# Kernel tuning notes

Measured on AMD Instinct MI355X. Metric: run time of the kernel, lower is better.

The kernel has to match this reference:

```python
import jax, jax.numpy as jnp
import numpy as np

N, FIN, FOUT = 4096, 256, 256


def setup_inputs() -> dict:
    key = jax.random.key(0)
    ks = jax.random.split(key, 6)
    x = jax.random.normal(ks[0], (N, FIN), jnp.float32)
    adj = jax.random.randint(ks[1], (N, N), 0, 2, jnp.int32)  # dense 0/1 adjacency
    W = jax.random.normal(ks[2], (FOUT, FIN), jnp.float32) / np.sqrt(FIN)
    b = jax.random.normal(ks[3], (FOUT,), jnp.float32) * 0.01
    att_w = jax.random.normal(ks[4], (2 * FOUT,), jnp.float32) / np.sqrt(2.0 * FOUT)  # Linear(2F,1).weight squeezed
    att_b = jax.random.normal(ks[5], (), jnp.float32) * 0.01
    return {"x": x, "adj": adj, "W": W, "b": b, "att_w": att_w, "att_b": att_b}


def reference(x, adj, W, b, att_w, att_b):
    n = x.shape[0]
    fo = W.shape[0]
    h = x @ W.T + b  # [N, Fout]
    # score(i,j) = att([h_i ; h_j]) = h_i.w1 + h_j.w2 + att_b  -> no [N,N,2F] concat
    s = (h @ att_w[:fo])[:, None] + (h @ att_w[fo:])[None, :] + att_b  # [N, N]
    edge = adj == 1
    # GLOBAL softmax over all edges (faithful to F.softmax(stacked_scores, dim=0))
    gmax = jnp.max(jnp.where(edge, s, -jnp.inf))
    e = jnp.exp(s - gmax)
    denom = jnp.sum(jnp.where(edge, e, 0.0))
    p = (e / denom).reshape(-1)  # softmaxed score per pair (valid at edges)
    # original indexes attention_scores[j] by NODE id j into the row-major edge list:
    # recover the score of the j-th global edge (j = 0..N-1) via cumsum rank + scatter
    flat = edge.reshape(-1)
    rank = jnp.cumsum(flat.astype(jnp.int32)) - 1  # rank of each edge in row-major order
    idx = jnp.where(flat, rank, n)  # non-edges and ranks >= n get dropped
    w_node = jnp.zeros((n,), h.dtype).at[idx].set(p, mode="drop")  # [N]
    # output[i] = sum_{j: adj[i,j]==1} w_node[j] * h[j]
    out = jax.nn.relu(edge.astype(h.dtype) @ (w_node[:, None] * h))
    return out
```

## Files before the change

### kernel.cpp

```cpp
#include <hip/hip_runtime.h>
#include <cstdint>
#include <cstddef>

#define NN 4096
#define FDIM 256

typedef __attribute__((ext_vector_type(4))) float fx4;
typedef __attribute__((ext_vector_type(8))) short s8v;

__device__ inline uint16_t f2bf(float f) {
    union { float f; uint32_t u; } v; v.f = f;
    const uint32_t u = v.u;
    return (uint16_t)((u + 0x7FFFu + ((u >> 16) & 1u)) >> 16);
}

__global__ __launch_bounds__(512, 4) void k_h(const float* __restrict__ x,
        const float* __restrict__ W, const float* __restrict__ bias,
        const float* __restrict__ att_w, uint16_t* __restrict__ gt,
        float* __restrict__ a1p, float* __restrict__ a2p) {
    __shared__ __align__(16) float xs[2][64 * 68];
    __shared__ __align__(16) float wt[2][64 * 68];
    const int bi = blockIdx.x, bf = blockIdx.y;
    const int t = threadIdx.x;
    const int t256 = t & 255;
    const int kh = t >> 8;
    const int tx = t256 & 15, ty = t256 >> 4;
    float acc[4][4] = {};
    float rx[8], rw[8];
    #pragma unroll
    for (int u = 0; u < 8; ++u) {
        const int e = t + 512 * u, r = e >> 6, c = e & 63;
        rx[u] = x[(size_t)(bi * 64 + r) * 256 + c];
        rw[u] = W[(size_t)(bf * 64 + r) * 256 + c];
    }
    for (int p = 0; p < 4; ++p) {
        float* xb = xs[p & 1];
        float* wb = wt[p & 1];
        #pragma unroll
        for (int u = 0; u < 8; ++u) {
            const int e = t + 512 * u, r = e >> 6, c = e & 63;
            const int sw = 8 * ((c & 7) ^ ((c >> 3) & 7));
            xb[c * 68 + (r ^ sw)] = rx[u];
            wb[c * 68 + (r ^ sw)] = rw[u];
        }
        __syncthreads();
        if (p < 3) {
            const int kc = (p + 1) * 64;
            #pragma unroll
            for (int u = 0; u < 8; ++u) {
                const int e = t + 512 * u, r = e >> 6, c = e & 63;
                rx[u] = x[(size_t)(bi * 64 + r) * 256 + kc + c];
                rw[u] = W[(size_t)(bf * 64 + r) * 256 + kc + c];
            }
        }
        #pragma unroll 8
        for (int k = 0; k < 32; ++k) {
            const int kk = kh * 32 + k;
            const int sw = 8 * ((kk & 7) ^ ((kk >> 3) & 7));
            const fx4 av = *(const fx4*)(xb + kk * 68 + ((ty * 4) ^ sw));
            const fx4 bv = *(const fx4*)(wb + kk * 68 + ((tx * 4) ^ sw));
            #pragma unroll
            for (int u = 0; u < 4; ++u)
                #pragma unroll
                for (int v = 0; v < 4; ++v)
                    acc[u][v] += av[u] * bv[v];
        }
    }
    __syncthreads();
    float* cbuf = xs[0];
    if (kh == 1) {
        #pragma unroll
        for (int u = 0; u < 4; ++u)
            *(fx4*)(cbuf + t256 * 16 + u * 4) = *(const fx4*)(&acc[u][0]);
    }
    __syncthreads();
    if (kh == 0) {
        float* tileT = wt[0];
        #pragma unroll
        for (int u = 0; u < 4; ++u) {
            const fx4 o = *(const fx4*)(cbuf + t256 * 16 + u * 4);
            #pragma unroll
            for (int v = 0; v < 4; ++v) acc[u][v] += o[v];
        }
        const fx4 bv = *(const fx4*)(bias + bf * 64 + tx * 4);
        const fx4 w1v = *(const fx4*)(att_w + bf * 64 + tx * 4);
        const fx4 w2v = *(const fx4*)(att_w + 256 + bf * 64 + tx * 4);
        #pragma unroll
        for (int u = 0; u < 4; ++u) {
            const int i = bi * 64 + ty * 4 + u;
            fx4 r;
            float s1 = 0.f, s2 = 0.f;
            #pragma unroll
            for (int v = 0; v < 4; ++v) {
                r[v] = acc[u][v] + bv[v];
                s1 += r[v] * w1v[v];
                s2 += r[v] * w2v[v];
            }
            #pragma unroll
            for (int v = 0; v < 4; ++v)
                tileT[(tx * 4 + v) * 68 + ty * 4 + u] = r[v];
            #pragma unroll
            for (int d = 8; d > 0; d >>= 1) {
                s1 += __shfl_down(s1, d, 16);
                s2 += __shfl_down(s2, d, 16);
            }
            if (tx == 0) {
                a1p[bf * NN + i] = s1;
                a2p[bf * NN + i] = s2;
            }
        }
    }
    __syncthreads();
    {
        const float* tileT = wt[0];
        const int fl = t >> 3, cb = t & 7;
        const int pcb = cb ^ (fl & 7);
        s8v v;
        #pragma unroll
        for (int lo = 0; lo < 8; ++lo)
            v[lo] = (short)f2bf(tileT[fl * 68 + cb * 8 + lo]);
        *(s8v*)(gt + (size_t)(bf * 64 + fl) * NN + bi * 64 + pcb * 8) = v;
    }
}

__global__ __launch_bounds__(1024) void k_prep(const float* __restrict__ a1p,
        const float* __restrict__ a2p, const int* __restrict__ adj,
        float* __restrict__ E1, float* __restrict__ E2,
        float* __restrict__ wraw, float* __restrict__ Sg) {
    __shared__ float E1s[NN];
    __shared__ float E2s[NN];
    __shared__ float red1[16], red2[16];
    __shared__ int wtot[16];
    __shared__ int base_s;
    const int t = threadIdx.x, lane = t & 63, wv = t >> 6;
    fx4 v1 = {0.f, 0.f, 0.f, 0.f}, v2 = {0.f, 0.f, 0.f, 0.f};
    #pragma unroll
    for (int bf = 0; bf < 4; ++bf) {
        v1 += *(const fx4*)(a1p + bf * NN + t * 4);
        v2 += *(const fx4*)(a2p + bf * NN + t * 4);
    }
    float m1 = fmaxf(fmaxf(v1[0], v1[1]), fmaxf(v1[2], v1[3]));
    float m2 = fmaxf(fmaxf(v2[0], v2[1]), fmaxf(v2[2], v2[3]));
    #pragma unroll
    for (int d = 32; d > 0; d >>= 1) {
        m1 = fmaxf(m1, __shfl_down(m1, d));
        m2 = fmaxf(m2, __shfl_down(m2, d));
    }
    if (lane == 0) { red1[wv] = m1; red2[wv] = m2; }
    __syncthreads();
    if (t == 0) {
        float mm1 = -1e30f, mm2 = -1e30f;
        for (int k = 0; k < 16; ++k) {
            mm1 = fmaxf(mm1, red1[k]);
            mm2 = fmaxf(mm2, red2[k]);
        }
        red1[0] = mm1; red2[0] = mm2;
        *Sg = 0.f;
        base_s = 0;
    }
    __syncthreads();
    const float M1 = red1[0], M2 = red2[0];
    fx4 e1v, e2v, z4 = {0.f, 0.f, 0.f, 0.f};
    #pragma unroll
    for (int j = 0; j < 4; ++j) {
        e1v[j] = expf(v1[j] - M1);
        e2v[j] = expf(v2[j] - M2);
    }
    *(fx4*)(E1s + t * 4) = e1v;
    *(fx4*)(E2s + t * 4) = e2v;
    *(fx4*)(E1 + t * 4) = e1v;
    *(fx4*)(E2 + t * 4) = e2v;
    *(fx4*)(wraw + t * 4) = z4;
    __syncthreads();
    for (int row = 0; row < NN; ++row) {
        const int base = base_s;
        if (base >= NN) break;
        const int4 a = ((const int4*)(adj + (size_t)row * NN))[t];
        const int vj[4] = {a.x, a.y, a.z, a.w};
        int cnt = 0;
        #pragma unroll
        for (int j = 0; j < 4; ++j) cnt += (vj[j] == 1);
        int inc = cnt;
        #pragma unroll
        for (int d = 1; d < 64; d <<= 1) {
            const int y = __shfl_up(inc, d);
            if (lane >= d) inc += y;
        }
        if (lane == 63) wtot[wv] = inc;
        __syncthreads();
        int wbase = 0, total = 0;
        #pragma unroll
        for (int w = 0; w < 16; ++w) {
            const int xw = wtot[w];
            total += xw;
            wbase += (w < wv) ? xw : 0;
        }
        if (t == 0) base_s = base + total;
        int r = base + wbase + inc - cnt;
        if (cnt && r < NN) {
            const float e1 = E1s[row];
            #pragma unroll
            for (int j = 0; j < 4; ++j) {
                if (vj[j] == 1) {
                    if (r < NN) wraw[r] = e1 * E2s[t * 4 + j];
                    ++r;
                }
            }
        }
        __syncthreads();
    }
}

__global__ __launch_bounds__(256, 3) void k_fused(const int* __restrict__ adj,
        const uint16_t* __restrict__ gt, const float* __restrict__ E1,
        const float* __restrict__ E2, const float* __restrict__ wraw,
        uint16_t* __restrict__ part, float* __restrict__ Sg, int krange) {
    __shared__ __align__(16) uint16_t As[64 * 72];
    __shared__ __align__(16) uint16_t Gs[256 * 64];
    __shared__ float sgred[4];
    const int ib = blockIdx.x, ks = blockIdx.y;
    const int t = threadIdx.x;
    const int wv = t >> 6, lane = t & 63;
    const int q = lane >> 4, m16 = lane & 15;
    const int i0 = ib * 64, k0 = ks * krange;
    const int ksteps = krange >> 6;
    const int ar = t >> 4, ac4 = (t & 15) * 4;
    const int fr = lane >> 3, cb = lane & 7;
    fx4 acc[4][4];
    #pragma unroll
    for (int a = 0; a < 4; ++a)
        #pragma unroll
        for (int b2 = 0; b2 < 4; ++b2) acc[a][b2] = (fx4){0.f, 0.f, 0.f, 0.f};
    float sS = 0.f;
    float e1r[4];
    #pragma unroll
    for (int p = 0; p < 4; ++p) e1r[p] = E1[i0 + p * 16 + ar];
    int4 ra[4];
    #pragma unroll
    for (int p = 0; p < 4; ++p)
        ra[p] = *(const int4*)(adj + (size_t)(i0 + p * 16 + ar) * NN + k0 + ac4);
    fx4 rw4 = *(const fx4*)(wraw + k0 + ac4);
    fx4 re2 = *(const fx4*)(E2 + k0 + ac4);

    for (int stp = 0; stp < ksteps; ++stp) {
        const int kk = k0 + stp * 64;
        const uint16_t wb0 = f2bf(rw4[0]), wb1 = f2bf(rw4[1]);
        const uint16_t wb2 = f2bf(rw4[2]), wb3 = f2bf(rw4[3]);
        #pragma unroll
        for (int p = 0; p < 4; ++p) {
            uint2 wo;
            wo.x = (ra[p].x == 1 ? (uint32_t)wb0 : 0u) |
                   ((ra[p].y == 1 ? (uint32_t)wb1 : 0u) << 16);
            wo.y = (ra[p].z == 1 ? (uint32_t)wb2 : 0u) |
                   ((ra[p].w == 1 ? (uint32_t)wb3 : 0u) << 16);
            *(uint2*)(&As[(p * 16 + ar) * 72 + ac4]) = wo;
            sS += e1r[p] * ((ra[p].x == 1 ? re2[0] : 0.f) +
                            (ra[p].y == 1 ? re2[1] : 0.f) +
                            (ra[p].z == 1 ? re2[2] : 0.f) +
                            (ra[p].w == 1 ? re2[3] : 0.f));
        }
        #pragma unroll
        for (int p = 0; p < 8; ++p) {
            const int f0 = wv * 64 + p * 8;
            const uint16_t* gp = gt + (size_t)(f0 + fr) * NN + kk + cb * 8;
            __builtin_amdgcn_global_load_lds(
                (const __attribute__((address_space(1))) uint32_t*)gp,
                (__attribute__((address_space(3))) uint32_t*)(Gs + f0 * 64),
                16, 0, 0);
        }
        __syncthreads();
        if (stp + 1 < ksteps) {
            #pragma unroll
            for (int p = 0; p < 4; ++p)
                ra[p] = *(const int4*)(adj + (size_t)(i0 + p * 16 + ar) * NN +
                                       kk + 64 + ac4);
            rw4 = *(const fx4*)(wraw + kk + 64 + ac4);
            re2 = *(const fx4*)(E2 + kk + 64 + ac4);
        }
        s8v afr[4][2];
        #pragma unroll
        for (int it = 0; it < 4; ++it)
            #pragma unroll
            for (int khh = 0; khh < 2; ++khh)
                afr[it][khh] = *(const s8v*)(As + (it * 16 + m16) * 72 + khh * 32 + q * 8);
        #pragma unroll
        for (int ft = 0; ft < 4; ++ft) {
            #pragma unroll
            for (int khh = 0; khh < 2; ++khh) {
                const int row = wv * 64 + ft * 16 + m16;
                const int pcb = ((khh << 2) | q) ^ (m16 & 7);
                const s8v bfr = *(const s8v*)(Gs + row * 64 + pcb * 8);
                #pragma unroll
                for (int it = 0; it < 4; ++it)
                    acc[it][ft] = __builtin_amdgcn_mfma_f32_16x16x32_bf16(
                        afr[it][khh], bfr, acc[it][ft], 0, 0, 0);
            }
        }
        __syncthreads();
    }
    #pragma unroll
    for (int d = 32; d > 0; d >>= 1) sS += __shfl_down(sS, d);
    if (lane == 0) sgred[wv] = sS;
    __syncthreads();
    if (t == 0)
        atomicAdd(Sg, sgred[0] + sgred[1] + sgred[2] + sgred[3]);
    uint16_t* dst = part + (size_t)ks * NN * FDIM;
    #pragma unroll
    for (int it = 0; it < 4; ++it) {
        #pragma unroll
        for (int ft = 0; ft < 4; ++ft) {
            const int f = wv * 64 + ft * 16 + m16;
            #pragma unroll
            for (int r = 0; r < 4; ++r) {
                const int i = i0 + it * 16 + q * 4 + r;
                dst[(size_t)i * FDIM + f] = f2bf(acc[it][ft][r]);
            }
        }
    }
}

__global__ __launch_bounds__(256) void k_out(const uint16_t* __restrict__ part,
        const float* __restrict__ Sg, float* __restrict__ out, int nsplit) {
    const size_t idx = ((size_t)blockIdx.x * 256 + threadIdx.x) * 8;
    const float inv = 1.0f / (*Sg);
    float s[8] = {};
    for (int k = 0; k < nsplit; ++k) {
        const s8v v = *(const s8v*)(part + (size_t)k * NN * FDIM + idx);
        #pragma unroll
        for (int j = 0; j < 8; ++j) {
            union { uint32_t u; float f; } cv;
            cv.u = ((uint32_t)(uint16_t)v[j]) << 16;
            s[j] += cv.f;
        }
    }
    fx4 r0, r1;
    #pragma unroll
    for (int j = 0; j < 4; ++j) {
        r0[j] = fmaxf(s[j], 0.f) * inv;
        r1[j] = fmaxf(s[4 + j], 0.f) * inv;
    }
    *(fx4*)(out + idx) = r0;
    *(fx4*)(out + idx + 4) = r1;
}

extern "C" void kernel_launch(void* const* d_in, const int* in_sizes, int n_in,
                              void* d_out, int out_size, void* d_ws, size_t ws_size,
                              hipStream_t stream) {
    const float* x     = (const float*)d_in[0];
    const int*   adj   = (const int*)d_in[1];
    const float* W     = (const float*)d_in[2];
    const float* bias  = (const float*)d_in[3];
    const float* att_w = (const float*)d_in[4];
    float* out = (float*)d_out;
    char* ws = (char*)d_ws;
    uint16_t* gt   = (uint16_t*)(ws + 0);
    float*    a1p  = (float*)(ws + 2097152);
    float*    a2p  = (float*)(ws + 2162688);
    float*    E1   = (float*)(ws + 2228224);
    float*    E2   = (float*)(ws + 2244608);
    float*    wraw = (float*)(ws + 2260992);
    float*    Sg   = (float*)(ws + 2277376);
    uint16_t* part = (uint16_t*)(ws + 2277632);
    (void)in_sizes; (void)n_in; (void)out_size;

    const size_t avail = (ws_size > 2277632) ? (ws_size - 2277632) : 0;
    int splitk = 1;
    while (splitk < 8 &&
           (size_t)(splitk * 2) * NN * FDIM * sizeof(uint16_t) <= avail)
        splitk <<= 1;
    const int krange = NN / splitk;

    k_h    <<<dim3(64, 4), 512, 0, stream>>>(x, W, bias, att_w, gt, a1p, a2p);
    k_prep <<<dim3(1), 1024, 0, stream>>>(a1p, a2p, adj, E1, E2, wraw, Sg);
    k_fused<<<dim3(64, splitk), 256, 0, stream>>>(adj, gt, E1, E2, wraw, part, Sg, krange);
    k_out  <<<dim3(512), 256, 0, stream>>>(part, Sg, out, splitk);
}
```

Measured before the change: 148.1 us.

## Load B operand directly into registers and double-buffer adjacency tile in LDS

The fused aggregation kernel stops staging the transposed feature tile through LDS via global_load_lds and instead loads each wave's B fragments straight from global memory into registers, prefetching the next step. The adjacency-weight A tile is double-buffered in LDS so the trailing barrier per step is removed, and adjacency rows are prefetched two steps ahead. The XOR swizzle on the gt writes is dropped since the LDS bank-conflict layout is no longer needed. This raises register pressure, so occupancy is lowered to 2 blocks per CU. It also assumes ksteps is even.

After: 153.2 us. 1.03x slower.

```diff
diff --git a/kernel.cpp b/kernel.cpp
--- a/kernel.cpp
+++ b/kernel.cpp
@@ -114,12 +114,11 @@
     {
         const float* tileT = wt[0];
         const int fl = t >> 3, cb = t & 7;
-        const int pcb = cb ^ (fl & 7);
         s8v v;
         #pragma unroll
         for (int lo = 0; lo < 8; ++lo)
             v[lo] = (short)f2bf(tileT[fl * 68 + cb * 8 + lo]);
-        *(s8v*)(gt + (size_t)(bf * 64 + fl) * NN + bi * 64 + pcb * 8) = v;
+        *(s8v*)(gt + (size_t)(bf * 64 + fl) * NN + bi * 64 + cb * 8) = v;
     }
 }
 
@@ -211,12 +210,11 @@
     }
 }
 
-__global__ __launch_bounds__(256, 3) void k_fused(const int* __restrict__ adj,
+__global__ __launch_bounds__(256, 2) void k_fused(const int* __restrict__ adj,
         const uint16_t* __restrict__ gt, const float* __restrict__ E1,
         const float* __restrict__ E2, const float* __restrict__ wraw,
         uint16_t* __restrict__ part, float* __restrict__ Sg, int krange) {
-    __shared__ __align__(16) uint16_t As[64 * 72];
-    __shared__ __align__(16) uint16_t Gs[256 * 64];
+    __shared__ __align__(16) uint16_t As[2][64 * 72];
     __shared__ float sgred[4];
     const int ib = blockIdx.x, ks = blockIdx.y;
     const int t = threadIdx.x;
@@ -225,7 +223,6 @@
     const int i0 = ib * 64, k0 = ks * krange;
     const int ksteps = krange >> 6;
     const int ar = t >> 4, ac4 = (t & 15) * 4;
-    const int fr = lane >> 3, cb = lane & 7;
     fx4 acc[4][4];
     #pragma unroll
     for (int a = 0; a < 4; ++a)
@@ -235,69 +232,83 @@
     float e1r[4];
     #pragma unroll
     for (int p = 0; p < 4; ++p) e1r[p] = E1[i0 + p * 16 + ar];
-    int4 ra[4];
+    const uint16_t* rowp[4];
+    #pragma unroll
+    for (int ft = 0; ft < 4; ++ft)
+        rowp[ft] = gt + (size_t)(wv * 64 + ft * 16 + m16) * NN + q * 8;
+
+    int4 ra0[4], ra1[4];
     #pragma unroll
     for (int p = 0; p < 4; ++p)
-        ra[p] = *(const int4*)(adj + (size_t)(i0 + p * 16 + ar) * NN + k0 + ac4);
-    fx4 rw4 = *(const fx4*)(wraw + k0 + ac4);
-    fx4 re2 = *(const fx4*)(E2 + k0 + ac4);
-
-    for (int stp = 0; stp < ksteps; ++stp) {
+        ra0[p] = *(const int4*)(adj + (size_t)(i0 + p * 16 + ar) * NN + k0 + ac4);
+    #pragma unroll
+    for (int p = 0; p < 4; ++p)
+        ra1[p] = *(const int4*)(adj + (size_t)(i0 + p * 16 + ar) * NN + k0 + 64 + ac4);
+    fx4 rwC = *(const fx4*)(wraw + k0 + ac4);
+    fx4 reC = *(const fx4*)(E2 + k0 + ac4);
+    s8v B0[4][2], B1[4][2];
+    #pragma unroll
+    for (int ft = 0; ft < 4; ++ft) {
+        B0[ft][0] = *(const s8v*)(rowp[ft] + k0);
+        B0[ft][1] = *(const s8v*)(rowp[ft] + k0 + 32);
+    }
+
+    auto step = [&](s8v (&Bc)[4][2], s8v (&Bn)[4][2], int4 (&Rc)[4], int stp) {
+        const int cur = stp & 1;
         const int kk = k0 + stp * 64;
-        const uint16_t wb0 = f2bf(rw4[0]), wb1 = f2bf(rw4[1]);
-        const uint16_t wb2 = f2bf(rw4[2]), wb3 = f2bf(rw4[3]);
+        const uint16_t wb0 = f2bf(rwC[0]), wb1 = f2bf(rwC[1]);
+        const uint16_t wb2 = f2bf(rwC[2]), wb3 = f2bf(rwC[3]);
         #pragma unroll
         for (int p = 0; p < 4; ++p) {
             uint2 wo;
-            wo.x = (ra[p].x == 1 ? (uint32_t)wb0 : 0u) |
-                   ((ra[p].y == 1 ? (uint32_t)wb1 : 0u) << 16);
-            wo.y = (ra[p].z == 1 ? (uint32_t)wb2 : 0u) |
-                   ((ra[p].w == 1 ? (uint32_t)wb3 : 0u) << 16);
-            *(uint2*)(&As[(p * 16 + ar) * 72 + ac4]) = wo;
-            sS += e1r[p] * ((ra[p].x == 1 ? re2[0] : 0.f) +
-                            (ra[p].y == 1 ? re2[1] : 0.f) +
-                            (ra[p].z == 1 ? re2[2] : 0.f) +
-                            (ra[p].w == 1 ? re2[3] : 0.f));
-        }
-        #pragma unroll
-        for (int p = 0; p < 8; ++p) {
-            const int f0 = wv * 64 + p * 8;
-            const uint16_t* gp = gt + (size_t)(f0 + fr) * NN + kk + cb * 8;
-            __builtin_amdgcn_global_load_lds(
-                (const __attribute__((address_space(1))) uint32_t*)gp,
-                (__attribute__((address_space(3))) uint32_t*)(Gs + f0 * 64),
-                16, 0, 0);
+            wo.x = (Rc[p].x == 1 ? (uint32_t)wb0 : 0u) |
+                   ((Rc[p].y == 1 ? (uint32_t)wb1 : 0u) << 16);
+            wo.y = (Rc[p].z == 1 ? (uint32_t)wb2 : 0u) |
+                   ((Rc[p].w == 1 ? (uint32_t)wb3 : 0u) << 16);
+            *(uint2*)(&As[cur][(p * 16 + ar) * 72 + ac4]) = wo;
+            sS += e1r[p] * ((Rc[p].x == 1 ? reC[0] : 0.f) +
+                            (Rc[p].y == 1 ? reC[1] : 0.f) +
+                            (Rc[p].z == 1 ? reC[2] : 0.f) +
+                            (Rc[p].w == 1 ? reC[3] : 0.f));
         }
         __syncthreads();
+        if (stp + 2 < ksteps) {
+            #pragma unroll
+            for (int p = 0; p < 4; ++p)
+                Rc[p] = *(const int4*)(adj + (size_t)(i0 + p * 16 + ar) * NN +
+                                       kk + 128 + ac4);
+        }
         if (stp + 1 < ksteps) {
-            #pragma unroll
-            for (int p = 0; p < 4; ++p)
-                ra[p] = *(const int4*)(adj + (size_t)(i0 + p * 16 + ar) * NN +
-                                       kk + 64 + ac4);
-            rw4 = *(const fx4*)(wraw + kk + 64 + ac4);
-            re2 = *(const fx4*)(E2 + kk + 64 + ac4);
+            rwC = *(const fx4*)(wraw + kk + 64 + ac4);
+            reC = *(const fx4*)(E2 + kk + 64 + ac4);
+            #pragma unroll
+            for (int ft = 0; ft < 4; ++ft) {
+                Bn[ft][0] = *(const s8v*)(rowp[ft] + kk + 64);
+                Bn[ft][1] = *(const s8v*)(rowp[ft] + kk + 64 + 32);
+            }
         }
         s8v afr[4][2];
         #pragma unroll
         for (int it = 0; it < 4; ++it)
             #pragma unroll
             for (int khh = 0; khh < 2; ++khh)
-                afr[it][khh] = *(const s8v*)(As + (it * 16 + m16) * 72 + khh * 32 + q * 8);
-        #pragma unroll
-        for (int ft = 0; ft < 4; ++ft) {
-            #pragma unroll
-            for (int khh = 0; khh < 2; ++khh) {
-                const int row = wv * 64 + ft * 16 + m16;
-                const int pcb = ((khh << 2) | q) ^ (m16 & 7);
-                const s8v bfr = *(const s8v*)(Gs + row * 64 + pcb * 8);
+                afr[it][khh] = *(const s8v*)(&As[cur][(it * 16 + m16) * 72 +
+                                                      khh * 32 + q * 8]);
+        #pragma unroll
+        for (int ft = 0; ft < 4; ++ft)
+            #pragma unroll
+            for (int khh = 0; khh < 2; ++khh)
                 #pragma unroll
                 for (int it = 0; it < 4; ++it)
                     acc[it][ft] = __builtin_amdgcn_mfma_f32_16x16x32_bf16(
-                        afr[it][khh], bfr, acc[it][ft], 0, 0, 0);
-            }
-        }
-        __syncthreads();
-    }
+                        afr[it][khh], Bc[ft][khh], acc[it][ft], 0, 0, 0);
+    };
+
+    for (int stp = 0; stp < ksteps; stp += 2) {
+        step(B0, B1, ra0, stp);
+        step(B1, B0, ra1, stp + 1);
+    }
+
     #pragma unroll
     for (int d = 32; d > 0; d >>= 1) sS += __shfl_down(sS, d);
     if (lane == 0) sgred[wv] = sS;
```

## Fuse single-block prep kernel into split-K fused kernel with redundant per-block edge ranking

Applied to the files above, without the earlier changes.

Removes the single-block k_prep kernel, which serially scanned adjacency rows to build the node weight vector. Each k_fused block now recomputes the global maxima, E1/E2 exponentials and its own slice of edge-rank weights in shared memory, stopping once enough edges have been counted. This removes a serial launch that used one block on the device. In exchange, every block redundantly scans early adjacency rows and reduces a1p/a2p, and the split-K factor is now fixed at 8 with no workspace-size check.

New measurement: 154.2 us. +4.1%, slower.

```diff
diff --git a/kernel.cpp b/kernel.cpp
--- a/kernel.cpp
+++ b/kernel.cpp
@@ -4,6 +4,9 @@
 
 #define NN 4096
 #define FDIM 256
+#define SPLITK 8
+#define KRANGE 512
+#define KSTEPS 8
 
 typedef __attribute__((ext_vector_type(4))) float fx4;
 typedef __attribute__((ext_vector_type(8))) short s8v;
@@ -17,7 +20,7 @@
 __global__ __launch_bounds__(512, 4) void k_h(const float* __restrict__ x,
         const float* __restrict__ W, const float* __restrict__ bias,
         const float* __restrict__ att_w, uint16_t* __restrict__ gt,
-        float* __restrict__ a1p, float* __restrict__ a2p) {
+        float* __restrict__ a1p, float* __restrict__ a2p, float* __restrict__ Sg) {
     __shared__ __align__(16) float xs[2][64 * 68];
     __shared__ __align__(16) float wt[2][64 * 68];
     const int bi = blockIdx.x, bf = blockIdx.y;
@@ -25,6 +28,7 @@
     const int t256 = t & 255;
     const int kh = t >> 8;
     const int tx = t256 & 15, ty = t256 >> 4;
+    if (bi == 0 && bf == 0 && t == 0) *Sg = 0.f;
     float acc[4][4] = {};
     float rx[8], rw[8];
     #pragma unroll
@@ -123,136 +127,140 @@
     }
 }
 
-__global__ __launch_bounds__(1024) void k_prep(const float* __restrict__ a1p,
-        const float* __restrict__ a2p, const int* __restrict__ adj,
-        float* __restrict__ E1, float* __restrict__ E2,
-        float* __restrict__ wraw, float* __restrict__ Sg) {
-    __shared__ float E1s[NN];
-    __shared__ float E2s[NN];
-    __shared__ float red1[16], red2[16];
-    __shared__ int wtot[16];
-    __shared__ int base_s;
-    const int t = threadIdx.x, lane = t & 63, wv = t >> 6;
-    fx4 v1 = {0.f, 0.f, 0.f, 0.f}, v2 = {0.f, 0.f, 0.f, 0.f};
-    #pragma unroll
-    for (int bf = 0; bf < 4; ++bf) {
-        v1 += *(const fx4*)(a1p + bf * NN + t * 4);
-        v2 += *(const fx4*)(a2p + bf * NN + t * 4);
-    }
-    float m1 = fmaxf(fmaxf(v1[0], v1[1]), fmaxf(v1[2], v1[3]));
-    float m2 = fmaxf(fmaxf(v2[0], v2[1]), fmaxf(v2[2], v2[3]));
-    #pragma unroll
-    for (int d = 32; d > 0; d >>= 1) {
-        m1 = fmaxf(m1, __shfl_down(m1, d));
-        m2 = fmaxf(m2, __shfl_down(m2, d));
-    }
-    if (lane == 0) { red1[wv] = m1; red2[wv] = m2; }
-    __syncthreads();
-    if (t == 0) {
-        float mm1 = -1e30f, mm2 = -1e30f;
-        for (int k = 0; k < 16; ++k) {
-            mm1 = fmaxf(mm1, red1[k]);
-            mm2 = fmaxf(mm2, red2[k]);
-        }
-        red1[0] = mm1; red2[0] = mm2;
-        *Sg = 0.f;
-        base_s = 0;
-    }
-    __syncthreads();
-    const float M1 = red1[0], M2 = red2[0];
-    fx4 e1v, e2v, z4 = {0.f, 0.f, 0.f, 0.f};
-    #pragma unroll
-    for (int j = 0; j < 4; ++j) {
-        e1v[j] = expf(v1[j] - M1);
-        e2v[j] = expf(v2[j] - M2);
-    }
-    *(fx4*)(E1s + t * 4) = e1v;
-    *(fx4*)(E2s + t * 4) = e2v;
-    *(fx4*)(E1 + t * 4) = e1v;
-    *(fx4*)(E2 + t * 4) = e2v;
-    *(fx4*)(wraw + t * 4) = z4;
-    __syncthreads();
-    for (int row = 0; row < NN; ++row) {
-        const int base = base_s;
-        if (base >= NN) break;
-        const int4 a = ((const int4*)(adj + (size_t)row * NN))[t];
-        const int vj[4] = {a.x, a.y, a.z, a.w};
-        int cnt = 0;
-        #pragma unroll
-        for (int j = 0; j < 4; ++j) cnt += (vj[j] == 1);
-        int inc = cnt;
-        #pragma unroll
-        for (int d = 1; d < 64; d <<= 1) {
-            const int y = __shfl_up(inc, d);
-            if (lane >= d) inc += y;
-        }
-        if (lane == 63) wtot[wv] = inc;
-        __syncthreads();
-        int wbase = 0, total = 0;
-        #pragma unroll
-        for (int w = 0; w < 16; ++w) {
-            const int xw = wtot[w];
-            total += xw;
-            wbase += (w < wv) ? xw : 0;
-        }
-        if (t == 0) base_s = base + total;
-        int r = base + wbase + inc - cnt;
-        if (cnt && r < NN) {
-            const float e1 = E1s[row];
-            #pragma unroll
-            for (int j = 0; j < 4; ++j) {
-                if (vj[j] == 1) {
-                    if (r < NN) wraw[r] = e1 * E2s[t * 4 + j];
-                    ++r;
-                }
-            }
-        }
-        __syncthreads();
-    }
-}
-
 __global__ __launch_bounds__(256, 3) void k_fused(const int* __restrict__ adj,
-        const uint16_t* __restrict__ gt, const float* __restrict__ E1,
-        const float* __restrict__ E2, const float* __restrict__ wraw,
-        uint16_t* __restrict__ part, float* __restrict__ Sg, int krange) {
+        const uint16_t* __restrict__ gt, const float* __restrict__ a1p,
+        const float* __restrict__ a2p, uint16_t* __restrict__ part,
+        float* __restrict__ Sg) {
     __shared__ __align__(16) uint16_t As[64 * 72];
     __shared__ __align__(16) uint16_t Gs[256 * 64];
+    __shared__ __align__(16) float E2w[KRANGE];
+    __shared__ __align__(16) uint16_t wbf[KRANGE];
+    __shared__ float mred[8];
+    __shared__ int wtot[4];
     __shared__ float sgred[4];
     const int ib = blockIdx.x, ks = blockIdx.y;
     const int t = threadIdx.x;
     const int wv = t >> 6, lane = t & 63;
     const int q = lane >> 4, m16 = lane & 15;
-    const int i0 = ib * 64, k0 = ks * krange;
-    const int ksteps = krange >> 6;
+    const int i0 = ib * 64, k0 = ks * KRANGE;
     const int ar = t >> 4, ac4 = (t & 15) * 4;
     const int fr = lane >> 3, cb = lane & 7;
+
+    {
+        float lm1 = -1e30f, lm2 = -1e30f;
+        #pragma unroll
+        for (int j = 0; j < 4; ++j) {
+            const int idx = t * 16 + j * 4;
+            fx4 s1 = *(const fx4*)(a1p + idx);
+            fx4 s2 = *(const fx4*)(a2p + idx);
+            #pragma unroll
+            for (int c = 1; c < 4; ++c) {
+                s1 += *(const fx4*)(a1p + c * NN + idx);
+                s2 += *(const fx4*)(a2p + c * NN + idx);
+            }
+            lm1 = fmaxf(lm1, fmaxf(fmaxf(s1[0], s1[1]), fmaxf(s1[2], s1[3])));
+            lm2 = fmaxf(lm2, fmaxf(fmaxf(s2[0], s2[1]), fmaxf(s2[2], s2[3])));
+        }
+        #pragma unroll
+        for (int d = 32; d > 0; d >>= 1) {
+            lm1 = fmaxf(lm1, __shfl_down(lm1, d));
+            lm2 = fmaxf(lm2, __shfl_down(lm2, d));
+        }
+        if (lane == 0) { mred[wv] = lm1; mred[4 + wv] = lm2; }
+    }
+    __syncthreads();
+    const float M1 = fmaxf(fmaxf(mred[0], mred[1]), fmaxf(mred[2], mred[3]));
+    const float M2 = fmaxf(fmaxf(mred[4], mred[5]), fmaxf(mred[6], mred[7]));
+    #pragma unroll
+    for (int j = 0; j < 2; ++j) {
+        const int c = k0 + t * 2 + j;
+        float a2s = a2p[c];
+        a2s += a2p[NN + c]; a2s += a2p[2 * NN + c]; a2s += a2p[3 * NN + c];
+        E2w[t * 2 + j] = expf(a2s - M2);
+        wbf[t * 2 + j] = 0;
+    }
+    float e1r[4];
+    #pragma unroll
+    for (int p = 0; p < 4; ++p) {
+        const int i = i0 + p * 16 + ar;
+        float a1s = a1p[i];
+        a1s += a1p[NN + i]; a1s += a1p[2 * NN + i]; a1s += a1p[3 * NN + i];
+        e1r[p] = expf(a1s - M1);
+    }
+    __syncthreads();
+    {
+        const int kend = k0 + KRANGE;
+        int base = 0;
+        for (int row = 0; row < NN && base < kend; ++row) {
+            const int4* ap = (const int4*)(adj + (size_t)row * NN) + t * 4;
+            const int4 a0 = ap[0], a1v = ap[1], a2v = ap[2], a3v = ap[3];
+            const int va[16] = {a0.x, a0.y, a0.z, a0.w, a1v.x, a1v.y, a1v.z, a1v.w,
+                                a2v.x, a2v.y, a2v.z, a2v.w, a3v.x, a3v.y, a3v.z, a3v.w};
+            int cnt = 0;
+            #pragma unroll
+            for (int j = 0; j < 16; ++j) cnt += (va[j] == 1);
+            int inc = cnt;
+            #pragma unroll
+            for (int d = 1; d < 64; d <<= 1) {
+                const int y = __shfl_up(inc, d);
+                if (lane >= d) inc += y;
+            }
+            if (lane == 63) wtot[wv] = inc;
+            __syncthreads();
+            int wbase = 0, total = 0;
+            #pragma unroll
+            for (int w = 0; w < 4; ++w) {
+                const int xw = wtot[w];
+                total += xw;
+                wbase += (w < wv) ? xw : 0;
+            }
+            int r = base + wbase + inc - cnt;
+            if (cnt && r < kend && r + cnt > k0) {
+                float a1s = a1p[row];
+                a1s += a1p[NN + row]; a1s += a1p[2 * NN + row]; a1s += a1p[3 * NN + row];
+                const float e1row = expf(a1s - M1);
+                #pragma unroll
+                for (int j = 0; j < 16; ++j) {
+                    if (va[j] == 1) {
+                        if (r >= k0 && r < kend) {
+                            const int col = t * 16 + j;
+                            float a2s = a2p[col];
+                            a2s += a2p[NN + col]; a2s += a2p[2 * NN + col];
+                            a2s += a2p[3 * NN + col];
+                            wbf[r - k0] = f2bf(e1row * expf(a2s - M2));
+                        }
+                        ++r;
+                    }
+                }
+            }
+            base += total;
+            __syncthreads();
+        }
+    }
+    __syncthreads();
+
     fx4 acc[4][4];
     #pragma unroll
     for (int a = 0; a < 4; ++a)
         #pragma unroll
         for (int b2 = 0; b2 < 4; ++b2) acc[a][b2] = (fx4){0.f, 0.f, 0.f, 0.f};
     float sS = 0.f;
-    float e1r[4];
-    #pragma unroll
-    for (int p = 0; p < 4; ++p) e1r[p] = E1[i0 + p * 16 + ar];
     int4 ra[4];
     #pragma unroll
     for (int p = 0; p < 4; ++p)
         ra[p] = *(const int4*)(adj + (size_t)(i0 + p * 16 + ar) * NN + k0 + ac4);
-    fx4 rw4 = *(const fx4*)(wraw + k0 + ac4);
-    fx4 re2 = *(const fx4*)(E2 + k0 + ac4);
-
-    for (int stp = 0; stp < ksteps; ++stp) {
+
+    for (int stp = 0; stp < KSTEPS; ++stp) {
         const int kk = k0 + stp * 64;
-        const uint16_t wb0 = f2bf(rw4[0]), wb1 = f2bf(rw4[1]);
-        const uint16_t wb2 = f2bf(rw4[2]), wb3 = f2bf(rw4[3]);
+        const uint2 ww = *(const uint2*)(&wbf[stp * 64 + ac4]);
+        const fx4 re2 = *(const fx4*)(&E2w[stp * 64 + ac4]);
         #pragma unroll
         for (int p = 0; p < 4; ++p) {
             uint2 wo;
-            wo.x = (ra[p].x == 1 ? (uint32_t)wb0 : 0u) |
-                   ((ra[p].y == 1 ? (uint32_t)wb1 : 0u) << 16);
-            wo.y = (ra[p].z == 1 ? (uint32_t)wb2 : 0u) |
-                   ((ra[p].w == 1 ? (uint32_t)wb3 : 0u) << 16);
+            wo.x = ww.x & ((ra[p].x == 1 ? 0xFFFFu : 0u) |
+                           (ra[p].y == 1 ? 0xFFFF0000u : 0u));
+            wo.y = ww.y & ((ra[p].z == 1 ? 0xFFFFu : 0u) |
+                           (ra[p].w == 1 ? 0xFFFF0000u : 0u));
             *(uint2*)(&As[(p * 16 + ar) * 72 + ac4]) = wo;
             sS += e1r[p] * ((ra[p].x == 1 ? re2[0] : 0.f) +
                             (ra[p].y == 1 ? re2[1] : 0.f) +
@@ -269,13 +277,11 @@
                 16, 0, 0);
         }
         __syncthreads();
-        if (stp + 1 < ksteps) {
+        if (stp + 1 < KSTEPS) {
             #pragma unroll
             for (int p = 0; p < 4; ++p)
                 ra[p] = *(const int4*)(adj + (size_t)(i0 + p * 16 + ar) * NN +
                                        kk + 64 + ac4);
-            rw4 = *(const fx4*)(wraw + kk + 64 + ac4);
-            re2 = *(const fx4*)(E2 + kk + 64 + ac4);
         }
         s8v afr[4][2];
         #pragma unroll
@@ -320,11 +326,11 @@
 }
 
 __global__ __launch_bounds__(256) void k_out(const uint16_t* __restrict__ part,
-        const float* __restrict__ Sg, float* __restrict__ out, int nsplit) {
+        const float* __restrict__ Sg, float* __restrict__ out) {
     const size_t idx = ((size_t)blockIdx.x * 256 + threadIdx.x) * 8;
     const float inv = 1.0f / (*Sg);
     float s[8] = {};
-    for (int k = 0; k < nsplit; ++k) {
+    for (int k = 0; k < SPLITK; ++k) {
         const s8v v = *(const s8v*)(part + (size_t)k * NN * FDIM + idx);
         #pragma unroll
         for (int j = 0; j < 8; ++j) {
@@ -356,22 +362,11 @@
     uint16_t* gt   = (uint16_t*)(ws + 0);
     float*    a1p  = (float*)(ws + 2097152);
     float*    a2p  = (float*)(ws + 2162688);
-    float*    E1   = (float*)(ws + 2228224);
-    float*    E2   = (float*)(ws + 2244608);
-    float*    wraw = (float*)(ws + 2260992);
-    float*    Sg   = (float*)(ws + 2277376);
-    uint16_t* part = (uint16_t*)(ws + 2277632);
-    (void)in_sizes; (void)n_in; (void)out_size;
-
-    const size_t avail = (ws_size > 2277632) ? (ws_size - 2277632) : 0;
-    int splitk = 1;
-    while (splitk < 8 &&
-           (size_t)(splitk * 2) * NN * FDIM * sizeof(uint16_t) <= avail)
-        splitk <<= 1;
-    const int krange = NN / splitk;
-
-    k_h    <<<dim3(64, 4), 512, 0, stream>>>(x, W, bias, att_w, gt, a1p, a2p);
-    k_prep <<<dim3(1), 1024, 0, stream>>>(a1p, a2p, adj, E1, E2, wraw, Sg);
-    k_fused<<<dim3(64, splitk), 256, 0, stream>>>(adj, gt, E1, E2, wraw, part, Sg, krange);
-    k_out  <<<dim3(512), 256, 0, stream>>>(part, Sg, out, splitk);
-}
+    float*    Sg   = (float*)(ws + 2228224);
+    uint16_t* part = (uint16_t*)(ws + 2228480);
+    (void)in_sizes; (void)n_in; (void)out_size; (void)ws_size;
+
+    k_h    <<<dim3(64, 4), 512, 0, stream>>>(x, W, bias, att_w, gt, a1p, a2p, Sg);
+    k_fused<<<dim3(64, SPLITK), 256, 0, stream>>>(adj, gt, a1p, a2p, part, Sg);
+    k_out  <<<dim3(512), 256, 0, stream>>>(part, Sg, out);
+}
```
